# Optimization experiments

Measured on AMD Instinct MI355X. Metric: run time of the kernel, lower is better.

The kernel has to match this reference:

```python
import jax, jax.numpy as jnp
import numpy as np

B, N, F_IN, F_OUT, H, R = 8, 1024, 512, 512, 8, 16
HD = F_OUT // H


def fake_quant(x):
    """Simulated symmetric int8 quantize->dequantize (per-tensor)."""
    scale = jnp.maximum(jnp.max(jnp.abs(x)) / 127.0, 1e-8)
    q = jnp.clip(jnp.round(x / scale), -127.0, 127.0) * scale
    # straight-through estimator so the same fn works under vjp
    return x + jax.lax.stop_gradient(q - x)


def dora_linear(x, W, A, Bm, mag):
    """DoRA-merged linear: W' = mag * (W + B@A) / ||W + B@A||_row; y = x @ W'.T"""
    Wd = W + Bm @ A                                  # (out, in)
    col_norm = jnp.linalg.norm(Wd, axis=1, keepdims=True)  # (out, 1)
    Wp = (mag[:, None] / col_norm) * Wd
    return x @ Wp.T


def setup_inputs() -> dict:
    key = jax.random.key(0)
    ks = jax.random.split(key, 14)
    s = 0.02
    d = {
        "x": jax.random.normal(ks[0], (B, N, F_IN), jnp.float32),
        "adj_matrix": jax.random.randint(ks[1], (B, N, N), 0, 2, jnp.int32),
    }
    for i, nm in enumerate(["q", "k", "v"]):
        d[f"W_{nm}"] = jax.random.normal(ks[2 + 4 * i], (F_OUT, F_IN), jnp.float32) * s
        d[f"A_{nm}"] = jax.random.normal(ks[3 + 4 * i], (R, F_IN), jnp.float32) * s
        d[f"B_{nm}"] = jax.random.normal(ks[4 + 4 * i], (F_OUT, R), jnp.float32) * s
        d[f"m_{nm}"] = jnp.ones((F_OUT,), jnp.float32)
    return d


def reference(x, adj_matrix, W_q, A_q, B_q, m_q, W_k, A_k, B_k, m_k, W_v, A_v, B_v, m_v):
    bs, n, _ = x.shape
    # DoRA-merged Q/K/V projections -> (b, h, n, hd)
    def split_heads(t):
        return t.reshape(bs, n, H, HD).transpose(0, 2, 1, 3)
    q = split_heads(dora_linear(x, W_q, A_q, B_q, m_q))
    k = split_heads(dora_linear(x, W_k, A_k, B_k, m_k))
    v = split_heads(dora_linear(x, W_v, A_v, B_v, m_v))
    # quantized_matmul: quantize operands, dense dot-product scores (no 1/sqrt(d) in source)
    scores = jnp.einsum("bhnd,bhmd->bhnm", fake_quant(q), fake_quant(k))
    # adjacency masking: attn.masked_fill(adj == 0, -inf)
    scores = jnp.where(adj_matrix[:, None, :, :] == 0, -1e9, scores)
    # quantized_softmax + dequantize (dropout is identity in eval)
    attn = fake_quant(jax.nn.softmax(scores, axis=-1))  # (b, h, n, n)
    out = jnp.einsum("bhnm,bhmd->bhnd", attn, v)         # (b, h, n, hd)
    out = out.transpose(0, 2, 1, 3).reshape(bs, n, F_OUT)
    return out, attn
```

## Files before the change

kernel.cpp:

```cpp
#include <hip/hip_runtime.h>
#include <math.h>


typedef __attribute__((ext_vector_type(8))) short short8;
typedef __attribute__((ext_vector_type(4))) float floatx4;

#define OB_WPT   0ull
#define OB_XT    4718592ull
#define OB_VT    OB_XT
#define OB_QRAW  36700160ull
#define OB_PS    OB_QRAW
#define OB_KRAW  53477376ull
#define OB_VRAW  70254592ull
#define OB_QLV   70254592ull
#define OB_KLV   78643200ull
#define OB_RS    87031808ull
#define OB_BM    87556096ull
#define OB_AMAX  88604672ull

__device__ __forceinline__ unsigned short bf16_rne(float f) {
    unsigned int u = __float_as_uint(f);
    unsigned int r = u + 0x7fffu + ((u >> 16) & 1u);
    return (unsigned short)(r >> 16);
}
__device__ __forceinline__ float bf16_to_f(unsigned short h) {
    return __uint_as_float(((unsigned int)h) << 16);
}
__device__ __forceinline__ unsigned short bf16_exact(float f) {
    return (unsigned short)(__float_as_uint(f) >> 16);
}

__device__ __forceinline__ void dma16u(const unsigned short* g, unsigned short* l) {
    __builtin_amdgcn_global_load_lds(
        (__attribute__((address_space(1))) void*)(void*)g,
        (__attribute__((address_space(3))) void*)(void*)l, 16, 0, 0);
}

__global__ __launch_bounds__(256) void adj_bits_k(
    const int* __restrict__ adj, unsigned long long* __restrict__ bm)
{
    int tid = threadIdx.x;
    int wv = tid >> 6, lane = tid & 63;
    size_t word = (size_t)blockIdx.x * 4 + wv;
    int a = adj[word * 64 + lane];
    unsigned long long m = __ballot(a != 0);
    if (lane == 0) bm[word] = m;
}

__global__ __launch_bounds__(256) void splitx_k(
    const float* __restrict__ x, unsigned short* __restrict__ xh,
    unsigned short* __restrict__ xm, unsigned short* __restrict__ xl)
{
    int i = blockIdx.x * 256 + threadIdx.x;
    float4 v = ((const float4*)x)[i];
    ushort4 h, m, l;
    float r1, r2;
    h.x = bf16_rne(v.x); r1 = v.x - bf16_to_f(h.x);
    m.x = bf16_rne(r1);  r2 = r1 - bf16_to_f(m.x);  l.x = bf16_rne(r2);
    h.y = bf16_rne(v.y); r1 = v.y - bf16_to_f(h.y);
    m.y = bf16_rne(r1);  r2 = r1 - bf16_to_f(m.y);  l.y = bf16_rne(r2);
    h.z = bf16_rne(v.z); r1 = v.z - bf16_to_f(h.z);
    m.z = bf16_rne(r1);  r2 = r1 - bf16_to_f(m.z);  l.z = bf16_rne(r2);
    h.w = bf16_rne(v.w); r1 = v.w - bf16_to_f(h.w);
    m.w = bf16_rne(r1);  r2 = r1 - bf16_to_f(m.w);  l.w = bf16_rne(r2);
    ((ushort4*)xh)[i] = h;
    ((ushort4*)xm)[i] = m;
    ((ushort4*)xl)[i] = l;
}

__global__ __launch_bounds__(256) void build_wp3_k(
    const float* __restrict__ W_q, const float* __restrict__ A_q,
    const float* __restrict__ B_q, const float* __restrict__ m_q,
    const float* __restrict__ W_k, const float* __restrict__ A_k,
    const float* __restrict__ B_k, const float* __restrict__ m_k,
    const float* __restrict__ W_v, const float* __restrict__ A_v,
    const float* __restrict__ B_v, const float* __restrict__ m_v,
    unsigned short* __restrict__ wph, unsigned short* __restrict__ wpm,
    unsigned short* __restrict__ wpl)
{
    __shared__ float brow[16];
    __shared__ __align__(16) float wd[512];
    __shared__ float red[5];
    int o = blockIdx.x;
    int mtx = blockIdx.y;
    const float* W   = mtx == 0 ? W_q : (mtx == 1 ? W_k : W_v);
    const float* A   = mtx == 0 ? A_q : (mtx == 1 ? A_k : A_v);
    const float* Bm  = mtx == 0 ? B_q : (mtx == 1 ? B_k : B_v);
    const float* mag = mtx == 0 ? m_q : (mtx == 1 ? m_k : m_v);
    int ocol = mtx * 512 + o;
    int tid = threadIdx.x;
    if (tid < 16) brow[tid] = Bm[o * 16 + tid];
    __syncthreads();
    float ss = 0.f;
    for (int i = tid; i < 512; i += 256) {
        float acc = W[o * 512 + i];
#pragma unroll
        for (int r = 0; r < 16; ++r) acc = fmaf(brow[r], A[r * 512 + i], acc);
        wd[i] = acc;
        ss = fmaf(acc, acc, ss);
    }
#pragma unroll
    for (int off = 32; off > 0; off >>= 1) ss += __shfl_down(ss, off);
    int lane = tid & 63, wv = tid >> 6;
    if (lane == 0) red[wv] = ss;
    __syncthreads();
    if (tid == 0) red[4] = mag[o] / sqrtf(red[0] + red[1] + red[2] + red[3]);
    __syncthreads();
    float scl = red[4];
    for (int i = tid; i < 512; i += 256) {
        float v = wd[i] * scl;
        unsigned short h = bf16_rne(v);
        float r1 = v - bf16_to_f(h);
        unsigned short m = bf16_rne(r1);
        float r2 = r1 - bf16_to_f(m);
        wph[(size_t)ocol * 512 + i] = h;
        wpm[(size_t)ocol * 512 + i] = m;
        wpl[(size_t)ocol * 512 + i] = bf16_rne(r2);
    }
}

__global__ __launch_bounds__(256) void proj_mfma_k(
    const unsigned short* __restrict__ xh, const unsigned short* __restrict__ xm,
    const unsigned short* __restrict__ xl,
    const unsigned short* __restrict__ wph, const unsigned short* __restrict__ wpm,
    const unsigned short* __restrict__ wpl,
    float* __restrict__ qraw, float* __restrict__ kraw, float* __restrict__ vraw,
    unsigned int* __restrict__ amax)
{
    __shared__ __align__(16) unsigned short Ah[128][32];
    __shared__ __align__(16) unsigned short Am[128][32];
    __shared__ __align__(16) unsigned short Al[128][32];
    __shared__ __align__(16) unsigned short Bh[128][32];
    __shared__ __align__(16) unsigned short Bmd[128][32];
    __shared__ __align__(16) unsigned short Bl[128][32];
    __shared__ float redmax[4];
    int tid = threadIdx.x;
    int lane = tid & 63, w = tid >> 6;
    int g = blockIdx.y * 64 + blockIdx.x;
    int xcd = g & 7, slot = g >> 3;
    int tt = (xcd << 3) | (slot / 12);
    int oo = slot - (slot / 12) * 12;
    int t0 = tt * 128;
    int o0 = oo * 128;
    int mtx = o0 >> 9;
    float* dst = mtx == 0 ? qraw : (mtx == 1 ? kraw : vraw);
    int wt0 = (w >> 1) * 64;
    int wo0 = (w & 1) * 64;

    floatx4 acc[4][4];
#pragma unroll
    for (int mi = 0; mi < 4; ++mi)
#pragma unroll
        for (int nj = 0; nj < 4; ++nj) acc[mi][nj] = (floatx4){0.f, 0.f, 0.f, 0.f};

    int srow = w * 32 + (lane >> 2);
    int scol = (lane & 3) * 8;
    const unsigned short* gAh = xh  + (size_t)(t0 + srow) * 512 + scol;
    const unsigned short* gAm = xm  + (size_t)(t0 + srow) * 512 + scol;
    const unsigned short* gAl = xl  + (size_t)(t0 + srow) * 512 + scol;
    const unsigned short* gBh = wph + (size_t)(o0 + srow) * 512 + scol;
    const unsigned short* gBm = wpm + (size_t)(o0 + srow) * 512 + scol;
    const unsigned short* gBl = wpl + (size_t)(o0 + srow) * 512 + scol;

    int fr = lane & 15;
    int fk = (lane >> 4) * 8;

    for (int kt = 0; kt < 16; ++kt) {
        size_t ko = (size_t)kt * 32;
        dma16u(gAh + ko,            &Ah[w * 32][0]);
        dma16u(gAh + ko + 16 * 512, &Ah[w * 32 + 16][0]);
        dma16u(gAm + ko,            &Am[w * 32][0]);
        dma16u(gAm + ko + 16 * 512, &Am[w * 32 + 16][0]);
        dma16u(gAl + ko,            &Al[w * 32][0]);
        dma16u(gAl + ko + 16 * 512, &Al[w * 32 + 16][0]);
        dma16u(gBh + ko,            &Bh[w * 32][0]);
        dma16u(gBh + ko + 16 * 512, &Bh[w * 32 + 16][0]);
        dma16u(gBm + ko,            &Bmd[w * 32][0]);
        dma16u(gBm + ko + 16 * 512, &Bmd[w * 32 + 16][0]);
        dma16u(gBl + ko,            &Bl[w * 32][0]);
        dma16u(gBl + ko + 16 * 512, &Bl[w * 32 + 16][0]);
        __syncthreads();

        short8 ah[4], am[4], al[4];
#pragma unroll
        for (int mi = 0; mi < 4; ++mi) {
            int ar = wt0 + mi * 16 + fr;
            ah[mi] = *(const short8*)&Ah[ar][fk];
            am[mi] = *(const short8*)&Am[ar][fk];
            al[mi] = *(const short8*)&Al[ar][fk];
        }
#pragma unroll
        for (int nj = 0; nj < 4; ++nj) {
            int br = wo0 + nj * 16 + fr;
            short8 bh = *(const short8*)&Bh[br][fk];
            short8 bm = *(const short8*)&Bmd[br][fk];
            short8 bl = *(const short8*)&Bl[br][fk];
#pragma unroll
            for (int mi = 0; mi < 4; ++mi) {
                acc[mi][nj] = __builtin_amdgcn_mfma_f32_16x16x32_bf16(ah[mi], bh, acc[mi][nj], 0, 0, 0);
                acc[mi][nj] = __builtin_amdgcn_mfma_f32_16x16x32_bf16(ah[mi], bm, acc[mi][nj], 0, 0, 0);
                acc[mi][nj] = __builtin_amdgcn_mfma_f32_16x16x32_bf16(am[mi], bh, acc[mi][nj], 0, 0, 0);
                acc[mi][nj] = __builtin_amdgcn_mfma_f32_16x16x32_bf16(ah[mi], bl, acc[mi][nj], 0, 0, 0);
                acc[mi][nj] = __builtin_amdgcn_mfma_f32_16x16x32_bf16(al[mi], bh, acc[mi][nj], 0, 0, 0);
                acc[mi][nj] = __builtin_amdgcn_mfma_f32_16x16x32_bf16(am[mi], bm, acc[mi][nj], 0, 0, 0);
            }
        }
        __syncthreads();
    }

    float mx = 0.f;
#pragma unroll
    for (int mi = 0; mi < 4; ++mi) {
#pragma unroll
        for (int r = 0; r < 4; ++r) {
            int t = t0 + wt0 + mi * 16 + (lane >> 4) * 4 + r;
            int b = t >> 10, n = t & 1023;
#pragma unroll
            for (int nj = 0; nj < 4; ++nj) {
                int o = o0 + wo0 + nj * 16 + fr;
                int h = (o >> 6) & 7, d = o & 63;
                float val = acc[mi][nj][r];
                dst[((size_t)(b * 8 + h) * 1024 + n) * 64 + d] = val;
                mx = fmaxf(mx, fabsf(val));
            }
        }
    }
    if (mtx < 2) {
#pragma unroll
        for (int off = 32; off > 0; off >>= 1) mx = fmaxf(mx, __shfl_down(mx, off));
        if ((tid & 63) == 0) redmax[tid >> 6] = mx;
        __syncthreads();
        if (tid == 0) {
            float m2 = fmaxf(fmaxf(redmax[0], redmax[1]), fmaxf(redmax[2], redmax[3]));
            atomicMax(&amax[mtx], __float_as_uint(m2));
        }
    }
}

__global__ __launch_bounds__(256) void quant2_k(
    const float* __restrict__ qraw, const float* __restrict__ kraw,
    const unsigned int* __restrict__ amax,
    unsigned short* __restrict__ qlv, unsigned short* __restrict__ klv)
{
    int m = blockIdx.y;
    const float* raw = m ? kraw : qraw;
    unsigned short* lv = m ? klv : qlv;
    float scale = fmaxf(__uint_as_float(amax[m]) / 127.f, 1e-8f);
    int i = blockIdx.x * 256 + threadIdx.x;
    float4 v = ((const float4*)raw)[i];
    float l0 = fminf(fmaxf(rintf(v.x / scale), -127.f), 127.f);
    float l1 = fminf(fmaxf(rintf(v.y / scale), -127.f), 127.f);
    float l2 = fminf(fmaxf(rintf(v.z / scale), -127.f), 127.f);
    float l3 = fminf(fmaxf(rintf(v.w / scale), -127.f), 127.f);
    ushort4 o;
    o.x = bf16_exact(l0); o.y = bf16_exact(l1);
    o.z = bf16_exact(l2); o.w = bf16_exact(l3);
    ((ushort4*)lv)[i] = o;
}

__global__ __launch_bounds__(256) void vtrans_k(
    const float* __restrict__ vb, unsigned short* __restrict__ vt)
{
    __shared__ float ls[64][69];
    int tid = threadIdx.x;
    int mt = blockIdx.x, bh = blockIdx.y;
#pragma unroll
    for (int l = 0; l < 4; ++l) {
        int idx = l * 256 + tid;
        int r = idx >> 4, c4 = idx & 15;
        float4 v = *(const float4*)(vb + (size_t)(bh * 1024 + mt * 64 + r) * 64 + c4 * 4);
        ls[r][c4 * 4 + 0] = v.x; ls[r][c4 * 4 + 1] = v.y;
        ls[r][c4 * 4 + 2] = v.z; ls[r][c4 * 4 + 3] = v.w;
    }
    __syncthreads();
#pragma unroll
    for (int l = 0; l < 4; ++l) {
        int idx = l * 256 + tid;
        int d = idx >> 4, mg = idx & 15;
        ushort4 hi;
        hi.x = bf16_rne(ls[mg * 4 + 0][d]);
        hi.y = bf16_rne(ls[mg * 4 + 1][d]);
        hi.z = bf16_rne(ls[mg * 4 + 2][d]);
        hi.w = bf16_rne(ls[mg * 4 + 3][d]);
        *(ushort4*)(vt + (size_t)(bh * 64 + d) * 1024 + mt * 64 + mg * 4) = hi;
    }
}

__global__ __launch_bounds__(256) void attn_stats_k(
    const unsigned short* __restrict__ qlv, const unsigned short* __restrict__ klv,
    const unsigned long long* __restrict__ bm, const unsigned int* __restrict__ amax,
    float2* __restrict__ psums)
{
    int tid = threadIdx.x;
    int lane = tid & 63, w = tid >> 6;
    int m_ = lane & 15, quad = lane >> 4;
    int g = blockIdx.z * 1024 + blockIdx.y * 16 + blockIdx.x;
    int xcd = g & 7, slot = g >> 3;
    int bh = (xcd << 3) | (slot >> 6);
    int rem = slot & 63;
    int qt = rem >> 2, qtr = rem & 3;
    int b = bh >> 3;
    int rowbase = qt * 64 + w * 16;
    float sq = fmaxf(__uint_as_float(amax[0]) / 127.f, 1e-8f);
    float sk = fmaxf(__uint_as_float(amax[1]) / 127.f, 1e-8f);
    float ss = sq * sk;

    const unsigned short* qp = qlv + ((size_t)bh * 1024 + rowbase + m_) * 64;
    short8 Aq0 = *(const short8*)(qp + quad * 8);
    short8 Aq1 = *(const short8*)(qp + 32 + quad * 8);
    const unsigned short* kbase = klv + (size_t)bh * 1024 * 64;
    const unsigned long long* bmb = bm + ((size_t)b * 1024 + rowbase) * 16;

    float mrun[4], lrun[4];
#pragma unroll
    for (int r = 0; r < 4; ++r) { mrun[r] = -1e9f; lrun[r] = 0.f; }

    for (int ci = 0; ci < 4; ++ci) {
        int c = qtr * 4 + ci;
        unsigned long long mk[4];
#pragma unroll
        for (int r = 0; r < 4; ++r) mk[r] = bmb[(quad * 4 + r) * 16 + c];
        float sv[4][4];
#pragma unroll
        for (int s = 0; s < 4; ++s) {
            const unsigned short* kp = kbase + (size_t)(c * 64 + s * 16 + m_) * 64;
            short8 B0 = *(const short8*)(kp + quad * 8);
            short8 B1 = *(const short8*)(kp + 32 + quad * 8);
            floatx4 Cv = {0.f, 0.f, 0.f, 0.f};
            Cv = __builtin_amdgcn_mfma_f32_16x16x32_bf16(Aq0, B0, Cv, 0, 0, 0);
            Cv = __builtin_amdgcn_mfma_f32_16x16x32_bf16(Aq1, B1, Cv, 0, 0, 0);
            int colbit = s * 16 + m_;
#pragma unroll
            for (int r = 0; r < 4; ++r)
                sv[r][s] = ((mk[r] >> colbit) & 1ull) ? Cv[r] * ss : -1e9f;
        }
#pragma unroll
        for (int r = 0; r < 4; ++r) {
            float tm = fmaxf(fmaxf(sv[r][0], sv[r][1]), fmaxf(sv[r][2], sv[r][3]));
            float mn = fmaxf(mrun[r], tm);
            float e = __expf(sv[r][0] - mn) + __expf(sv[r][1] - mn)
                    + __expf(sv[r][2] - mn) + __expf(sv[r][3] - mn);
            lrun[r] = fmaf(lrun[r], __expf(mrun[r] - mn), e);
            mrun[r] = mn;
        }
    }

#pragma unroll
    for (int r = 0; r < 4; ++r) {
        float m = mrun[r], l = lrun[r];
#pragma unroll
        for (int off = 1; off < 16; off <<= 1) {
            float mo = __shfl_xor(m, off);
            float lo = __shfl_xor(l, off);
            float mn = fmaxf(m, mo);
            l = l * __expf(m - mn) + lo * __expf(mo - mn);
            m = mn;
        }
        if (m_ == 0)
            psums[(size_t)qtr * 65536 + (size_t)bh * 1024 + rowbase + quad * 4 + r] =
                make_float2(m, l);
    }
}

__global__ __launch_bounds__(256) void stats_merge_k(
    const float2* __restrict__ ps, float2* __restrict__ rowstats,
    unsigned int* __restrict__ amax_attn)
{
    int row = blockIdx.x * 256 + threadIdx.x;
    float2 a = ps[row];
    float m = a.x, l = a.y;
#pragma unroll
    for (int q = 1; q < 4; ++q) {
        float2 bq = ps[(size_t)q * 65536 + row];
        float mn = fmaxf(m, bq.x);
        l = l * __expf(m - mn) + bq.y * __expf(bq.x - mn);
        m = mn;
    }
    rowstats[row] = make_float2(m, l);
    float inv = 1.0f / l;
#pragma unroll
    for (int off = 1; off < 64; off <<= 1) inv = fmaxf(inv, __shfl_xor(inv, off));
    if ((threadIdx.x & 63) == 0) atomicMax(amax_attn, __float_as_uint(inv));
}

__global__ __launch_bounds__(256) void attn_out_k(
    const unsigned short* __restrict__ qlv, const unsigned short* __restrict__ klv,
    const unsigned short* __restrict__ vt,
    const unsigned long long* __restrict__ bm, const unsigned int* __restrict__ amax,
    const float2* __restrict__ rowstats,
    float* __restrict__ attn, float* __restrict__ out)
{
    __shared__ unsigned short pl[4][2][16][68];
    int tid = threadIdx.x;
    int lane = tid & 63, w = tid >> 6;
    int m_ = lane & 15, quad = lane >> 4;
    int g = blockIdx.y * 16 + blockIdx.x;
    int xcd = g & 7, slot = g >> 3;
    int bh = (xcd << 3) | (slot >> 4);
    int qt = slot & 15;
    int b = bh >> 3, h = bh & 7;
    int rowbase = qt * 64 + w * 16;
    float sq = fmaxf(__uint_as_float(amax[0]) / 127.f, 1e-8f);
    float sk = fmaxf(__uint_as_float(amax[1]) / 127.f, 1e-8f);
    float ss = sq * sk;
    float sa = fmaxf(__uint_as_float(amax[2]) / 127.f, 1e-8f);
    float inv_sa = 1.0f / sa;

    const unsigned short* qp = qlv + ((size_t)bh * 1024 + rowbase + m_) * 64;
    short8 Aq0 = *(const short8*)(qp + quad * 8);
    short8 Aq1 = *(const short8*)(qp + 32 + quad * 8);
    const unsigned short* kbase = klv + (size_t)bh * 1024 * 64;
    const unsigned long long* bmb = bm + ((size_t)b * 1024 + rowbase) * 16;

    float mrow[4], rlr[4];
#pragma unroll
    for (int r = 0; r < 4; ++r) {
        float2 st = rowstats[(size_t)bh * 1024 + rowbase + quad * 4 + r];
        mrow[r] = st.x;
        rlr[r] = 1.0f / st.y;
    }
    floatx4 acc[4];
#pragma unroll
    for (int r = 0; r < 4; ++r) acc[r] = (floatx4){0.f, 0.f, 0.f, 0.f};

    float* attn_b = attn + ((size_t)bh << 20);

    for (int ci = 0; ci < 16; ++ci) {
        int c = ci;
        short8 Vb0[4], Vb1[4];
#pragma unroll
        for (int dt = 0; dt < 4; ++dt) {
            const unsigned short* vp = vt + ((size_t)(bh * 64 + dt * 16 + m_)) * 1024 + c * 64;
            Vb0[dt] = *(const short8*)(vp + quad * 8);
            Vb1[dt] = *(const short8*)(vp + 32 + quad * 8);
        }
        unsigned long long mk[4];
#pragma unroll
        for (int r = 0; r < 4; ++r) mk[r] = bmb[(quad * 4 + r) * 16 + c];
        unsigned short* plw = &pl[w][ci & 1][0][0];
#pragma unroll
        for (int s = 0; s < 4; ++s) {
            const unsigned short* kp = kbase + (size_t)(c * 64 + s * 16 + m_) * 64;
            short8 B0 = *(const short8*)(kp + quad * 8);
            short8 B1 = *(const short8*)(kp + 32 + quad * 8);
            floatx4 Cv = {0.f, 0.f, 0.f, 0.f};
            Cv = __builtin_amdgcn_mfma_f32_16x16x32_bf16(Aq0, B0, Cv, 0, 0, 0);
            Cv = __builtin_amdgcn_mfma_f32_16x16x32_bf16(Aq1, B1, Cv, 0, 0, 0);
            int colbit = s * 16 + m_;
#pragma unroll
            for (int r = 0; r < 4; ++r) {
                float sval = ((mk[r] >> colbit) & 1ull) ? Cv[r] * ss : -1e9f;
                float p = __expf(sval - mrow[r]) * rlr[r];
                float lv = fminf(rintf(p * inv_sa), 127.f);
                plw[(quad * 4 + r) * 68 + colbit] = bf16_exact(lv);
            }
        }
        __asm__ volatile("s_waitcnt lgkmcnt(0)" ::: "memory");
        short8 Ap0 = *(const short8*)&pl[w][ci & 1][m_][quad * 8];
        short8 Ap1 = *(const short8*)&pl[w][ci & 1][m_][32 + quad * 8];
#pragma unroll
        for (int dt = 0; dt < 4; ++dt) {
            acc[dt] = __builtin_amdgcn_mfma_f32_16x16x32_bf16(Ap0, Vb0[dt], acc[dt], 0, 0, 0);
            acc[dt] = __builtin_amdgcn_mfma_f32_16x16x32_bf16(Ap1, Vb1[dt], acc[dt], 0, 0, 0);
        }
#pragma unroll
        for (int it = 0; it < 4; ++it) {
            int rrow = it * 4 + quad, col = m_ * 4;
            uint2 pk = *(const uint2*)&pl[w][ci & 1][rrow][col];
            float4 av;
            av.x = bf16_to_f((unsigned short)(pk.x & 0xffff)) * sa;
            av.y = bf16_to_f((unsigned short)(pk.x >> 16)) * sa;
            av.z = bf16_to_f((unsigned short)(pk.y & 0xffff)) * sa;
            av.w = bf16_to_f((unsigned short)(pk.y >> 16)) * sa;
            *(float4*)(attn_b + (((size_t)(rowbase + rrow)) << 10) + c * 64 + col) = av;
        }
    }
#pragma unroll
    for (int dt = 0; dt < 4; ++dt)
#pragma unroll
        for (int r = 0; r < 4; ++r) {
            int n = rowbase + quad * 4 + r;
            int d = dt * 16 + m_;
            out[(size_t)(b * 1024 + n) * 512 + h * 64 + d] = acc[dt][r] * sa;
        }
}

extern "C" void kernel_launch(void* const* d_in, const int* in_sizes, int n_in,
                              void* d_out, int out_size, void* d_ws, size_t ws_size,
                              hipStream_t stream)
{
    (void)in_sizes; (void)n_in; (void)out_size; (void)ws_size;
    const float* x   = (const float*)d_in[0];
    const int*   adj = (const int*)d_in[1];
    const float* W_q = (const float*)d_in[2];
    const float* A_q = (const float*)d_in[3];
    const float* B_q = (const float*)d_in[4];
    const float* m_q = (const float*)d_in[5];
    const float* W_k = (const float*)d_in[6];
    const float* A_k = (const float*)d_in[7];
    const float* B_k = (const float*)d_in[8];
    const float* m_k = (const float*)d_in[9];
    const float* W_v = (const float*)d_in[10];
    const float* A_v = (const float*)d_in[11];
    const float* B_v = (const float*)d_in[12];
    const float* m_v = (const float*)d_in[13];

    char* ws = (char*)d_ws;
    unsigned short* wph = (unsigned short*)(ws + OB_WPT);
    unsigned short* wpm = (unsigned short*)(ws + OB_WPT + 1572864);
    unsigned short* wpl = (unsigned short*)(ws + OB_WPT + 3145728);
    unsigned short* xh  = (unsigned short*)(ws + OB_XT);
    unsigned short* xm  = (unsigned short*)(ws + OB_XT + 8388608);
    unsigned short* xl  = (unsigned short*)(ws + OB_XT + 16777216);
    float* qraw         = (float*)(ws + OB_QRAW);
    float* kraw         = (float*)(ws + OB_KRAW);
    float* vraw         = (float*)(ws + OB_VRAW);
    unsigned short* qlv = (unsigned short*)(ws + OB_QLV);
    unsigned short* klv = (unsigned short*)(ws + OB_KLV);
    unsigned short* vt  = (unsigned short*)(ws + OB_VT);
    float2* rowstats    = (float2*)(ws + OB_RS);
    float2* psums       = (float2*)(ws + OB_PS);
    unsigned long long* bmask = (unsigned long long*)(ws + OB_BM);
    unsigned int* amax  = (unsigned int*)(ws + OB_AMAX);

    float* out_base  = (float*)d_out;
    float* attn_base = out_base + 4194304;

    hipMemsetAsync(amax, 0, 16, stream);

    adj_bits_k<<<32768, 256, 0, stream>>>(adj, bmask);
    splitx_k<<<4096, 256, 0, stream>>>(x, xh, xm, xl);

    build_wp3_k<<<dim3(512, 3), 256, 0, stream>>>(W_q, A_q, B_q, m_q,
                                                  W_k, A_k, B_k, m_k,
                                                  W_v, A_v, B_v, m_v, wph, wpm, wpl);
    proj_mfma_k<<<dim3(64, 12), 256, 0, stream>>>(xh, xm, xl, wph, wpm, wpl,
                                                  qraw, kraw, vraw, amax);
    vtrans_k<<<dim3(16, 64), 256, 0, stream>>>(vraw, vt);
    quant2_k<<<dim3(4096, 2), 256, 0, stream>>>(qraw, kraw, amax, qlv, klv);

    attn_stats_k<<<dim3(16, 64, 4), 256, 0, stream>>>(qlv, klv, bmask, amax, psums);
    stats_merge_k<<<256, 256, 0, stream>>>(psums, rowstats, amax + 2);
    attn_out_k<<<dim3(16, 64), 256, 0, stream>>>(qlv, klv, vt, bmask, amax,
                                                 rowstats, attn_base, out_base);
}
```

Baseline: 636.5 us.

## Stage K and V tiles in LDS via double-buffered async copies with XOR swizzle

The attention stats and output kernels now stage each 64x64 K tile (and V tile in the output kernel) into shared memory using direct global-to-LDS copies with double buffering, instead of having each wave load K/V from global memory on its own. K and V are written pre-swizzled (XOR on 8-element groups) by the quant and transpose kernels, so LDS reads avoid bank conflicts. This removes redundant global loads across the four waves that share the same K/V tile. In exchange it adds a barrier and a full vmcnt wait every iteration, which also waits on the attn stores, and it uses more LDS per block.

```diff
diff --git a/kernel.cpp b/kernel.cpp
--- a/kernel.cpp
+++ b/kernel.cpp
@@ -255,7 +255,15 @@
     ushort4 o;
     o.x = bf16_exact(l0); o.y = bf16_exact(l1);
     o.z = bf16_exact(l2); o.w = bf16_exact(l3);
-    ((ushort4*)lv)[i] = o;
+    int idx4 = i;
+    if (m) {
+        int elem0 = i * 4;
+        int d0 = elem0 & 63;
+        int n = (elem0 >> 6) & 1023;
+        int dp = (d0 & 7) | ((((d0 >> 3) ^ n) & 7) << 3);
+        idx4 = (elem0 - d0 + dp) >> 2;
+    }
+    ((ushort4*)lv)[idx4] = o;
 }
 
 __global__ __launch_bounds__(256) void vtrans_k(
@@ -282,7 +290,9 @@
         hi.y = bf16_rne(ls[mg * 4 + 1][d]);
         hi.z = bf16_rne(ls[mg * 4 + 2][d]);
         hi.w = bf16_rne(ls[mg * 4 + 3][d]);
-        *(ushort4*)(vt + (size_t)(bh * 64 + d) * 1024 + mt * 64 + mg * 4) = hi;
+        int ml = mg * 4;
+        int mlp = (ml & 7) | ((((ml >> 3) ^ d) & 7) << 3);
+        *(ushort4*)(vt + (size_t)(bh * 64 + d) * 1024 + mt * 64 + mlp) = hi;
     }
 }
 
@@ -291,6 +301,7 @@
     const unsigned long long* __restrict__ bm, const unsigned int* __restrict__ amax,
     float2* __restrict__ psums)
 {
+    __shared__ __align__(16) unsigned short Ks[2][64][64];
     int tid = threadIdx.x;
     int lane = tid & 63, w = tid >> 6;
     int m_ = lane & 15, quad = lane >> 4;
@@ -308,24 +319,40 @@
     const unsigned short* qp = qlv + ((size_t)bh * 1024 + rowbase + m_) * 64;
     short8 Aq0 = *(const short8*)(qp + quad * 8);
     short8 Aq1 = *(const short8*)(qp + 32 + quad * 8);
-    const unsigned short* kbase = klv + (size_t)bh * 1024 * 64;
     const unsigned long long* bmb = bm + ((size_t)b * 1024 + rowbase) * 16;
 
+    const unsigned short* gK = klv + ((size_t)bh * 1024 + w * 16) * 64 + lane * 8;
+    int sw0 = ((quad ^ m_) & 7) << 3;
+    int sw1 = (((4 + quad) ^ m_) & 7) << 3;
+
     float mrun[4], lrun[4];
 #pragma unroll
     for (int r = 0; r < 4; ++r) { mrun[r] = -1e9f; lrun[r] = 0.f; }
+
+    {
+        size_t off = (size_t)(qtr * 4) * 4096;
+        dma16u(gK + off,       &Ks[0][w * 16][0]);
+        dma16u(gK + off + 512, &Ks[0][w * 16 + 8][0]);
+    }
+    __asm__ volatile("s_waitcnt vmcnt(0)" ::: "memory");
+    __builtin_amdgcn_s_barrier();
 
     for (int ci = 0; ci < 4; ++ci) {
         int c = qtr * 4 + ci;
+        int buf = ci & 1;
+        if (ci < 3) {
+            size_t off = (size_t)(c + 1) * 4096;
+            dma16u(gK + off,       &Ks[buf ^ 1][w * 16][0]);
+            dma16u(gK + off + 512, &Ks[buf ^ 1][w * 16 + 8][0]);
+        }
         unsigned long long mk[4];
 #pragma unroll
         for (int r = 0; r < 4; ++r) mk[r] = bmb[(quad * 4 + r) * 16 + c];
         float sv[4][4];
 #pragma unroll
         for (int s = 0; s < 4; ++s) {
-            const unsigned short* kp = kbase + (size_t)(c * 64 + s * 16 + m_) * 64;
-            short8 B0 = *(const short8*)(kp + quad * 8);
-            short8 B1 = *(const short8*)(kp + 32 + quad * 8);
+            short8 B0 = *(const short8*)&Ks[buf][s * 16 + m_][sw0];
+            short8 B1 = *(const short8*)&Ks[buf][s * 16 + m_][sw1];
             floatx4 Cv = {0.f, 0.f, 0.f, 0.f};
             Cv = __builtin_amdgcn_mfma_f32_16x16x32_bf16(Aq0, B0, Cv, 0, 0, 0);
             Cv = __builtin_amdgcn_mfma_f32_16x16x32_bf16(Aq1, B1, Cv, 0, 0, 0);
@@ -343,6 +370,8 @@
             lrun[r] = fmaf(lrun[r], __expf(mrun[r] - mn), e);
             mrun[r] = mn;
         }
+        __asm__ volatile("s_waitcnt vmcnt(0)" ::: "memory");
+        __builtin_amdgcn_s_barrier();
     }
 
 #pragma unroll
@@ -390,6 +419,8 @@
     const float2* __restrict__ rowstats,
     float* __restrict__ attn, float* __restrict__ out)
 {
+    __shared__ __align__(16) unsigned short Ks[2][64][64];
+    __shared__ __align__(16) unsigned short Vs[2][64][64];
     __shared__ unsigned short pl[4][2][16][68];
     int tid = threadIdx.x;
     int lane = tid & 63, w = tid >> 6;
@@ -409,8 +440,13 @@
     const unsigned short* qp = qlv + ((size_t)bh * 1024 + rowbase + m_) * 64;
     short8 Aq0 = *(const short8*)(qp + quad * 8);
     short8 Aq1 = *(const short8*)(qp + 32 + quad * 8);
-    const unsigned short* kbase = klv + (size_t)bh * 1024 * 64;
     const unsigned long long* bmb = bm + ((size_t)b * 1024 + rowbase) * 16;
+
+    const unsigned short* gK  = klv + ((size_t)bh * 1024 + w * 16) * 64 + lane * 8;
+    const unsigned short* gV  = vt + ((size_t)(bh * 64 + w * 16 + (lane >> 3))) * 1024 + (lane & 7) * 8;
+    const unsigned short* gV2 = gV + 8 * 1024;
+    int sw0 = ((quad ^ m_) & 7) << 3;
+    int sw1 = (((4 + quad) ^ m_) & 7) << 3;
 
     float mrow[4], rlr[4];
 #pragma unroll
@@ -425,14 +461,26 @@
 
     float* attn_b = attn + ((size_t)bh << 20);
 
+#define STG(bf, cc) do {                                                  \
+        dma16u(gK + (size_t)(cc) * 4096,       &Ks[bf][w * 16][0]);       \
+        dma16u(gK + (size_t)(cc) * 4096 + 512, &Ks[bf][w * 16 + 8][0]);   \
+        dma16u(gV + (cc) * 64,                 &Vs[bf][w * 16][0]);       \
+        dma16u(gV2 + (cc) * 64,                &Vs[bf][w * 16 + 8][0]);   \
+    } while (0)
+
+    STG(0, 0);
+    __asm__ volatile("s_waitcnt vmcnt(0)" ::: "memory");
+    __builtin_amdgcn_s_barrier();
+
     for (int ci = 0; ci < 16; ++ci) {
         int c = ci;
+        int buf = ci & 1;
+        if (ci + 1 < 16) STG(buf ^ 1, ci + 1);
         short8 Vb0[4], Vb1[4];
 #pragma unroll
         for (int dt = 0; dt < 4; ++dt) {
-            const unsigned short* vp = vt + ((size_t)(bh * 64 + dt * 16 + m_)) * 1024 + c * 64;
-            Vb0[dt] = *(const short8*)(vp + quad * 8);
-            Vb1[dt] = *(const short8*)(vp + 32 + quad * 8);
+            Vb0[dt] = *(const short8*)&Vs[buf][dt * 16 + m_][sw0];
+            Vb1[dt] = *(const short8*)&Vs[buf][dt * 16 + m_][sw1];
         }
         unsigned long long mk[4];
 #pragma unroll
@@ -440,9 +488,8 @@
         unsigned short* plw = &pl[w][ci & 1][0][0];
 #pragma unroll
         for (int s = 0; s < 4; ++s) {
-            const unsigned short* kp = kbase + (size_t)(c * 64 + s * 16 + m_) * 64;
-            short8 B0 = *(const short8*)(kp + quad * 8);
-            short8 B1 = *(const short8*)(kp + 32 + quad * 8);
+            short8 B0 = *(const short8*)&Ks[buf][s * 16 + m_][sw0];
+            short8 B1 = *(const short8*)&Ks[buf][s * 16 + m_][sw1];
             floatx4 Cv = {0.f, 0.f, 0.f, 0.f};
             Cv = __builtin_amdgcn_mfma_f32_16x16x32_bf16(Aq0, B0, Cv, 0, 0, 0);
             Cv = __builtin_amdgcn_mfma_f32_16x16x32_bf16(Aq1, B1, Cv, 0, 0, 0);
@@ -474,7 +521,10 @@
             av.w = bf16_to_f((unsigned short)(pk.y >> 16)) * sa;
             *(float4*)(attn_b + (((size_t)(rowbase + rrow)) << 10) + c * 64 + col) = av;
         }
-    }
+        __asm__ volatile("s_waitcnt vmcnt(0)" ::: "memory");
+        __builtin_amdgcn_s_barrier();
+    }
+#undef STG
 #pragma unroll
     for (int dt = 0; dt < 4; ++dt)
 #pragma unroll
```

New measurement: 531.8 us. -16.5%, faster.
